# Performance work log

Hardware: AMD Instinct MI355X
Metric: run time of the kernel (lower is better)

Reference implementation:

```python
import jax, jax.numpy as jnp
import numpy as np

HEADS = 16
DIM_HEAD = 64
SCALE = DIM_HEAD ** -0.5


def setup_inputs() -> dict:
    key = jax.random.key(0)
    ks = jax.random.split(key, 5)
    dim = 1024
    inner = HEADS * DIM_HEAD  # 1024
    x = jax.random.normal(ks[0], (2, 2048, dim), dtype=jnp.float32)
    # Linear weights stored as [in, out] so y = x @ W
    s = dim ** -0.5
    Wq = jax.random.normal(ks[1], (dim, inner), dtype=jnp.float32) * s
    Wk = jax.random.normal(ks[2], (dim, inner), dtype=jnp.float32) * s
    Wv = jax.random.normal(ks[3], (dim, inner), dtype=jnp.float32) * s
    Wo = jax.random.normal(ks[4], (inner, dim), dtype=jnp.float32) * s
    bo = jnp.zeros((dim,), dtype=jnp.float32)
    return {"x": x, "Wq": Wq, "Wk": Wk, "Wv": Wv, "Wo": Wo, "bo": bo}


def reference(x, Wq, Wk, Wv, Wo, bo):
    b, n, _ = x.shape
    def split_heads(t):  # [b, n, h*d] -> [b, h, n, d]
        return t.reshape(b, n, HEADS, DIM_HEAD).transpose(0, 2, 1, 3)
    q = split_heads(x @ Wq)
    k = split_heads(x @ Wk)
    v = split_heads(x @ Wv)
    sim = jnp.einsum('bhid,bhjd->bhij', q, k) * SCALE  # [b, h, n, n]
    attn = jax.nn.softmax(sim, axis=-1)
    out = jnp.einsum('bhij,bhjd->bhid', attn, v)  # [b, h, n, d]
    out = out.transpose(0, 2, 1, 3).reshape(b, n, HEADS * DIM_HEAD)
    return out @ Wo + bo
```

## Files before the change

kernel.cpp:

```cpp
#include <hip/hip_runtime.h>
#include <hip/hip_fp16.h>

typedef _Float16 f16;
typedef __attribute__((ext_vector_type(8))) _Float16 half8;
typedef __attribute__((ext_vector_type(2))) __fp16 fp16x2_native;
typedef __attribute__((ext_vector_type(4))) float floatx4;
typedef __attribute__((ext_vector_type(16))) float f32x16;
typedef __attribute__((ext_vector_type(4))) unsigned uint4v;
typedef __attribute__((ext_vector_type(2))) unsigned uint2v;

static constexpr int DIM = 1024;
static constexpr int SEQ = 2048;
static constexpr int DH = 64;
static constexpr int MTOT = 4096;

__device__ __forceinline__ float fexp2(float x) {
#if __has_builtin(__builtin_amdgcn_exp2f)
  return __builtin_amdgcn_exp2f(x);
#else
  return exp2f(x);
#endif
}

__device__ __forceinline__ unsigned pkrtz(float a, float b) {
  fp16x2_native h = __builtin_amdgcn_cvt_pkrtz(a, b);
  return __builtin_bit_cast(unsigned, h);
}

__device__ __forceinline__ void pl32swap(unsigned& a, unsigned& b) {
#if __has_builtin(__builtin_amdgcn_permlane32_swap)
  uint2v r = __builtin_amdgcn_permlane32_swap(a, b, false, false);
  a = r.x;
  b = r.y;
#else
  asm volatile("v_permlane32_swap_b32 %0, %1" : "+v"(a), "+v"(b));
#endif
}

__device__ __forceinline__ void gll16(const f16* g, f16* l) {
  auto gp = (__attribute__((address_space(1))) unsigned*)(uintptr_t)(const void*)g;
  auto lp = (__attribute__((address_space(3))) unsigned*)(uintptr_t)(void*)l;
  __builtin_amdgcn_global_load_lds(gp, lp, 16, 0, 0);
}

__global__ __launch_bounds__(256) void k_transpose(
    const float* __restrict__ Wq, const float* __restrict__ Wk,
    const float* __restrict__ Wv, const float* __restrict__ Wo,
    f16* __restrict__ wt)
{
  __shared__ float tile[32][33];
  const int z = blockIdx.z;
  const float* W = (z == 0) ? Wq : (z == 1) ? Wk : (z == 2) ? Wv : Wo;
  f16* out = wt + (size_t)z * DIM * DIM;
  const int tx = threadIdx.x, ty = threadIdx.y;
  const int x0 = blockIdx.x * 32, y0 = blockIdx.y * 32;
#pragma unroll
  for (int i = 0; i < 4; ++i)
    tile[ty + i * 8][tx] = W[(size_t)(y0 + ty + i * 8) * DIM + (x0 + tx)];
  __syncthreads();
#pragma unroll
  for (int i = 0; i < 4; ++i)
    out[(size_t)(x0 + ty + i * 8) * DIM + (y0 + tx)] = (f16)tile[tx][ty + i * 8];
}

__global__ __launch_bounds__(256) void k_xcast(
    const float* __restrict__ in, f16* __restrict__ out)
{
  const int i = blockIdx.x * 256 + threadIdx.x;
  const float4* p = (const float4*)in;
  float4 a = p[2 * i], b = p[2 * i + 1];
  half8 h = {(f16)a.x, (f16)a.y, (f16)a.z, (f16)a.w,
             (f16)b.x, (f16)b.y, (f16)b.z, (f16)b.w};
  *(half8*)(out + (size_t)i * 8) = h;
}

__global__ __launch_bounds__(256) void k_vtrans(
    const f16* __restrict__ vh, f16* __restrict__ vt)
{
  __shared__ f16 T[64][72];
  const int tid = threadIdx.x;
  const int nt = blockIdx.x, bh = blockIdx.y;
  const int b = bh >> 4, h = bh & 15;
  const int n0 = nt * 64;
  const f16* src = vh + (size_t)b * SEQ * DIM + (size_t)h * DH;
#pragma unroll
  for (int i = 0; i < 2; ++i) {
    const int n = (tid >> 3) + i * 32;
    const int cc = tid & 7;
    half8 v = *(const half8*)(src + (size_t)(n0 + n) * DIM + cc * 8);
#pragma unroll
    for (int j = 0; j < 8; ++j) T[cc * 8 + j][n] = v[j];
  }
  __syncthreads();
  f16* dst = vt + (size_t)bh * DH * SEQ;
#pragma unroll
  for (int i = 0; i < 2; ++i) {
    const int d = (tid >> 3) + i * 32;
    const int cc = tid & 7;
    half8 w = *(const half8*)&T[d][cc * 8];
    *(half8*)(dst + (size_t)d * SEQ + n0 + cc * 8) = w;
  }
}

template <bool OUT_F32>
__global__ __launch_bounds__(256) void k_gemm2(
    const f16* __restrict__ A, const f16* __restrict__ BT,
    void* __restrict__ Cptr, const float* __restrict__ bias,
    int M, int N, int K, size_t bt_zstride, size_t c_zstride)
{
  __shared__ f16 SB[2][8192];

  const int tid = threadIdx.x;
  const int lane = tid & 63;
  const int wid = tid >> 6;
  const int wr = (wid >> 1) * 64, wc = (wid & 1) * 64;
  const int li = lane & 15, lg = lane >> 4;

  const f16* BTz = BT + (size_t)blockIdx.z * bt_zstride;
  const int row0 = blockIdx.x * 128, col0 = blockIdx.y * 128;

  const int c0 = tid;
  const int c1 = 256 + tid;
  const f16* a0 = A + (size_t)(row0 + (c0 >> 2)) * K + (c0 & 3) * 8;
  const f16* a1 = A + (size_t)(row0 + (c1 >> 2)) * K + (c1 & 3) * 8;
  const f16* b0 = BTz + (size_t)(col0 + (c0 >> 2)) * K + (c0 & 3) * 8;
  const f16* b1 = BTz + (size_t)(col0 + (c1 >> 2)) * K + (c1 & 3) * 8;
  const int da0 = wid * 512, da1 = 2048 + wid * 512;

  const floatx4 zero4 = {0.f, 0.f, 0.f, 0.f};
  floatx4 acc[4][4];
#pragma unroll
  for (int m = 0; m < 4; ++m)
#pragma unroll
    for (int n = 0; n < 4; ++n) acc[m][n] = zero4;

  auto issue = [&](int buf) {
    gll16(a0, &SB[buf][da0]);
    gll16(a1, &SB[buf][da1]);
    gll16(b0, &SB[buf][4096 + da0]);
    gll16(b1, &SB[buf][4096 + da1]);
    a0 += 32; a1 += 32; b0 += 32; b1 += 32;
  };

  const int nstep = K >> 5;
  issue(0);

  auto step = [&](int buf, int t) {
    asm volatile("s_waitcnt vmcnt(0)" ::: "memory");
    __builtin_amdgcn_s_barrier();
    asm volatile("" ::: "memory");
    if (t + 1 < nstep) issue(buf ^ 1);
    const f16* As = &SB[buf][0];
    const f16* Bs = &SB[buf][4096];
    half8 af[4], bf[4];
#pragma unroll
    for (int m = 0; m < 4; ++m)
      af[m] = *(const half8*)&As[(wr + m * 16 + li) * 32 + lg * 8];
#pragma unroll
    for (int n = 0; n < 4; ++n)
      bf[n] = *(const half8*)&Bs[(wc + n * 16 + li) * 32 + lg * 8];
#pragma unroll
    for (int m = 0; m < 4; ++m)
#pragma unroll
      for (int n = 0; n < 4; ++n)
        acc[m][n] = __builtin_amdgcn_mfma_f32_16x16x32_f16(af[m], bf[n], acc[m][n], 0, 0, 0);
  };

  for (int t2 = 0; t2 < nstep; t2 += 2) {
    step(0, t2);
    step(1, t2 + 1);
  }

#pragma unroll
  for (int m = 0; m < 4; ++m)
#pragma unroll
    for (int n = 0; n < 4; ++n)
#pragma unroll
      for (int r = 0; r < 4; ++r) {
        const int row = row0 + wr + m * 16 + lg * 4 + r;
        const int col = col0 + wc + n * 16 + li;
        if constexpr (OUT_F32) {
          float* C = (float*)Cptr + (size_t)blockIdx.z * c_zstride;
          C[(size_t)row * N + col] = acc[m][n][r] + bias[col];
        } else {
          f16* C = (f16*)Cptr + (size_t)blockIdx.z * c_zstride;
          C[(size_t)row * N + col] = (f16)acc[m][n][r];
        }
      }
}

__global__ __launch_bounds__(512) void k_attn4(
    const f16* __restrict__ qh, const f16* __restrict__ kh,
    const f16* __restrict__ vt, f16* __restrict__ oh)
{
  __shared__ f16 KV[2][16384];
  __shared__ float bc[8][32];
  __shared__ float Lm[4][32], Ll[4][32], W0[4][32], W1[4][32];

  const int tid = threadIdx.x;
  const int lane = tid & 63;
  const int wid = tid >> 6;
  const int g = wid >> 2;
  const int sub = wid & 3;
  const int col = lane & 31;
  const int hi = lane >> 5;

  const int id = blockIdx.x;
  const int xcd = id & 7;
  const int j = id >> 3;
  const int bh = xcd * 4 + (j >> 4);
  const int qi = j & 15;
  const int b = bh >> 4, h = bh & 15;

  const int q0 = qi * 128 + sub * 32;
  const size_t xbase = (size_t)b * SEQ * DIM + (size_t)h * DH;
  const size_t vtbase = (size_t)bh * DH * SEQ;

  const float SC = 0.125f * 1.44269504089f;
  const float RTRAW = 8.0f / SC;

  const int lc = tid & 511;
  const int srow = lc >> 3;
  const int sw = ((lc & 7) ^ (srow & 7)) * 8;
  const f16* ks0 = kh + xbase + (size_t)srow * DIM + sw;
  const f16* ks1 = kh + xbase + (size_t)(1024 + srow) * DIM + sw;
  const f16* vs0 = vt + vtbase + (size_t)srow * SEQ + sw;
  const f16* vs1 = vt + vtbase + (size_t)srow * SEQ + 1024 + sw;

  auto issue = [&](int buf) {
    f16* B = &KV[buf][wid * 512];
    gll16(ks0, B);
    gll16(vs0, B + 4096);
    gll16(ks1, B + 8192);
    gll16(vs1, B + 12288);
    ks0 += 64 * DIM; ks1 += 64 * DIM; vs0 += 64; vs1 += 64;
  };

  half8 qb[4];
  {
    const f16* qrow = qh + xbase + (size_t)(q0 + col) * DIM;
#pragma unroll
    for (int s = 0; s < 4; ++s) qb[s] = *(const half8*)(qrow + s * 16 + hi * 8);
  }

  f32x16 o0 = {0, 0, 0, 0, 0, 0, 0, 0, 0, 0, 0, 0, 0, 0, 0, 0};
  f32x16 o1 = {0, 0, 0, 0, 0, 0, 0, 0, 0, 0, 0, 0, 0, 0, 0, 0};
  float m = -1e30f, lsum = 0.f;

  issue(0);

  auto tile = [&](int buf, int t) {
    asm volatile("s_waitcnt vmcnt(0)" ::: "memory");
    __builtin_amdgcn_s_barrier();
    asm volatile("" ::: "memory");
    if (t < 15) issue(buf ^ 1);
    const f16* Ks = &KV[buf][g * 8192];
    const f16* Vs = Ks + 4096;

#pragma unroll
    for (int kvs = 0; kvs < 2; ++kvs) {
      const int krow = kvs * 32 + col;
      f32x16 sacc = {0, 0, 0, 0, 0, 0, 0, 0, 0, 0, 0, 0, 0, 0, 0, 0};
      __builtin_amdgcn_s_setprio(1);
#pragma unroll
      for (int s = 0; s < 4; ++s) {
        const int cc = (2 * s + hi) ^ (krow & 7);
        half8 ka = *(const half8*)&Ks[krow * 64 + cc * 8];
        sacc = __builtin_amdgcn_mfma_f32_32x32x16_f16(ka, qb[s], sacc, 0, 0, 0);
      }
      __builtin_amdgcn_s_setprio(0);

      float x0 = fmaxf(fmaxf(sacc[0], sacc[1]), fmaxf(sacc[2], sacc[3]));
      float x1 = fmaxf(fmaxf(sacc[4], sacc[5]), fmaxf(sacc[6], sacc[7]));
      float x2 = fmaxf(fmaxf(sacc[8], sacc[9]), fmaxf(sacc[10], sacc[11]));
      float x3 = fmaxf(fmaxf(sacc[12], sacc[13]), fmaxf(sacc[14], sacc[15]));
      float smax = fmaxf(fmaxf(x0, x1), fmaxf(x2, x3));
      smax = fmaxf(smax, __shfl_xor(smax, 32));

      if (!__all(smax <= m + RTRAW)) {
        const float mn = fmaxf(m, smax);
        const float alpha = fexp2((m - mn) * SC);
        m = mn;
        lsum *= alpha;
        if (hi == 0) bc[wid][col] = alpha;
#pragma unroll
        for (int r = 0; r < 16; ++r) {
          const float a2 = bc[wid][(r & 3) + 8 * (r >> 2) + 4 * hi];
          o0[r] *= a2;
          o1[r] *= a2;
        }
      }

      const float mc = m * SC;
      float pw[16];
#pragma unroll
      for (int r = 0; r < 16; ++r) pw[r] = fexp2(fmaf(sacc[r], SC, -mc));
      float s0 = (pw[0] + pw[1]) + (pw[2] + pw[3]);
      float s1 = (pw[4] + pw[5]) + (pw[6] + pw[7]);
      float s2 = (pw[8] + pw[9]) + (pw[10] + pw[11]);
      float s3 = (pw[12] + pw[13]) + (pw[14] + pw[15]);
      float rs = (s0 + s1) + (s2 + s3);
      rs += __shfl_xor(rs, 32);
      lsum += rs;

      __builtin_amdgcn_s_setprio(1);
#pragma unroll
      for (int s2i = 0; s2i < 2; ++s2i) {
        const int rb = s2i * 8;
        unsigned X0 = pkrtz(pw[rb + 0], pw[rb + 1]);
        unsigned X1 = pkrtz(pw[rb + 2], pw[rb + 3]);
        unsigned Y0 = pkrtz(pw[rb + 4], pw[rb + 5]);
        unsigned Y1 = pkrtz(pw[rb + 6], pw[rb + 7]);
        pl32swap(X0, Y0);
        pl32swap(X1, Y1);
        const half8 paf = __builtin_bit_cast(half8, (uint4v){X0, X1, Y0, Y1});
        const int kc = kvs * 4 + s2i * 2 + hi;
#pragma unroll
        for (int dt = 0; dt < 2; ++dt) {
          const int vrow = dt * 32 + col;
          const int cc = kc ^ (vrow & 7);
          half8 vb = *(const half8*)&Vs[vrow * 64 + cc * 8];
          if (dt == 0)
            o0 = __builtin_amdgcn_mfma_f32_32x32x16_f16(paf, vb, o0, 0, 0, 0);
          else
            o1 = __builtin_amdgcn_mfma_f32_32x32x16_f16(paf, vb, o1, 0, 0, 0);
        }
      }
      __builtin_amdgcn_s_setprio(0);
    }
  };

  for (int t2 = 0; t2 < 16; t2 += 2) {
    tile(0, t2);
    tile(1, t2 + 1);
  }

  const float inv = 1.0f / lsum;
  if (hi == 0) bc[wid][col] = inv;
  if (g == 1) {
    if (hi == 0) { Lm[sub][col] = m; Ll[sub][col] = lsum; }
    f16* po = &KV[0][0] + sub * 2048;
#pragma unroll
    for (int r = 0; r < 16; ++r) {
      const int qr = (r & 3) + 8 * (r >> 2) + 4 * hi;
      const float iv = bc[wid][qr];
      po[qr * 64 + col] = (f16)(o0[r] * iv);
      po[qr * 64 + 32 + col] = (f16)(o1[r] * iv);
    }
  }
  __syncthreads();
  if (g == 0) {
    const float m1 = Lm[sub][col], l1 = Ll[sub][col];
    const float M = fmaxf(m, m1);
    const float e0 = fexp2((m - M) * SC);
    const float a0 = lsum * e0;
    const float a1 = l1 * fexp2((m1 - M) * SC);
    const float rden = 1.0f / (a0 + a1);
    const float c0 = e0 * rden;
    const float w1 = a1 * rden;
    if (hi == 0) { W0[sub][col] = c0; W1[sub][col] = w1; }
    const f16* po = &KV[0][0] + sub * 2048;
#pragma unroll
    for (int r = 0; r < 16; ++r) {
      const int qr = (r & 3) + 8 * (r >> 2) + 4 * hi;
      const float c0r = W0[sub][qr], w1r = W1[sub][qr];
      f16* orow = oh + xbase + (size_t)(q0 + qr) * DIM;
      orow[col] = (f16)(c0r * o0[r] + w1r * (float)po[qr * 64 + col]);
      orow[32 + col] = (f16)(c0r * o1[r] + w1r * (float)po[qr * 64 + 32 + col]);
    }
  }
}

extern "C" void kernel_launch(void* const* d_in, const int* in_sizes, int n_in,
                              void* d_out, int out_size, void* d_ws, size_t ws_size,
                              hipStream_t stream)
{
  const float* x  = (const float*)d_in[0];
  const float* Wq = (const float*)d_in[1];
  const float* Wk = (const float*)d_in[2];
  const float* Wv = (const float*)d_in[3];
  const float* Wo = (const float*)d_in[4];
  const float* bo = (const float*)d_in[5];

  char* ws = (char*)d_ws;
  f16* wt   = (f16*)ws;
  f16* qkvh = (f16*)(ws + (size_t)8 * 1024 * 1024);
  f16* ohp  = (f16*)(ws + (size_t)32 * 1024 * 1024);
  f16* vtb  = (f16*)(ws + (size_t)40 * 1024 * 1024);
  f16* xh   = ohp;

  k_transpose<<<dim3(32, 32, 4), dim3(32, 8), 0, stream>>>(Wq, Wk, Wv, Wo, wt);

  k_xcast<<<2048, 256, 0, stream>>>(x, xh);

  k_gemm2<false><<<dim3(32, 8, 3), 256, 0, stream>>>(
      xh, wt, qkvh, nullptr, MTOT, DIM, DIM,
      (size_t)DIM * DIM, (size_t)MTOT * DIM);

  k_vtrans<<<dim3(32, 32), 256, 0, stream>>>(
      qkvh + (size_t)2 * MTOT * DIM, vtb);

  k_attn4<<<512, 512, 0, stream>>>(
      qkvh, qkvh + (size_t)MTOT * DIM, vtb, ohp);

  k_gemm2<true><<<dim3(32, 8, 1), 256, 0, stream>>>(
      ohp, wt + (size_t)3 * DIM * DIM, d_out, bo, MTOT, DIM, DIM, 0, 0);
}
```

Baseline: 120.7 us.

## Batch QK MFMAs per tile and use a wave-uniform running max

Both 32-key QK^T MFMA chains of a tile are issued back to back before either softmax step, so the second chain's matrix work can overlap the exp and PV processing of the first. The running max becomes wave-uniform through a full xor-shuffle reduction, so the rescale multiplies by a scalar alpha and no longer goes through LDS. Exponentials are computed speculatively with the old max and recomputed only when the max grows, and the row-sum cross-half shuffle moves out of the loop to the end. In exchange it holds an extra accumulator (more VGPRs), and the coarser shared max may raise the rescale rate or lose a little precision.

```diff
diff --git a/kernel.cpp b/kernel.cpp
--- a/kernel.cpp
+++ b/kernel.cpp
@@ -189,7 +189,7 @@
       }
 }
 
-__global__ __launch_bounds__(512) void k_attn4(
+__global__ __launch_bounds__(512) void k_attn7(
     const f16* __restrict__ qh, const f16* __restrict__ kh,
     const f16* __restrict__ vt, f16* __restrict__ oh)
 {
@@ -245,9 +245,68 @@
 
   f32x16 o0 = {0, 0, 0, 0, 0, 0, 0, 0, 0, 0, 0, 0, 0, 0, 0, 0};
   f32x16 o1 = {0, 0, 0, 0, 0, 0, 0, 0, 0, 0, 0, 0, 0, 0, 0, 0};
-  float m = -1e30f, lsum = 0.f;
+  float m = -1e30f, mc = 0.f;
+  float lsum = 0.f;
 
   issue(0);
+
+  auto process = [&](const f32x16& sacc, int kvs, const f16* Vs) {
+    float pw[16];
+#pragma unroll
+    for (int r = 0; r < 16; ++r) pw[r] = fexp2(fmaf(sacc[r], SC, -mc));
+
+    float x0 = fmaxf(fmaxf(sacc[0], sacc[1]), fmaxf(sacc[2], sacc[3]));
+    float x1 = fmaxf(fmaxf(sacc[4], sacc[5]), fmaxf(sacc[6], sacc[7]));
+    float x2 = fmaxf(fmaxf(sacc[8], sacc[9]), fmaxf(sacc[10], sacc[11]));
+    float x3 = fmaxf(fmaxf(sacc[12], sacc[13]), fmaxf(sacc[14], sacc[15]));
+    const float smax = fmaxf(fmaxf(x0, x1), fmaxf(x2, x3));
+
+    if (!__all(smax <= m + RTRAW)) {
+      float wm = smax;
+#pragma unroll
+      for (int off = 1; off < 64; off <<= 1) wm = fmaxf(wm, __shfl_xor(wm, off));
+      const float mn = fmaxf(m, wm);
+      const float alpha = fexp2((m - mn) * SC);
+      m = mn;
+      mc = m * SC;
+      lsum *= alpha;
+#pragma unroll
+      for (int r = 0; r < 16; ++r) { o0[r] *= alpha; o1[r] *= alpha; }
+#pragma unroll
+      for (int r = 0; r < 16; ++r) pw[r] = fexp2(fmaf(sacc[r], SC, -mc));
+    }
+
+    float t0 = (pw[0] + pw[1]) + (pw[2] + pw[3]);
+    float t1 = (pw[4] + pw[5]) + (pw[6] + pw[7]);
+    float t2 = (pw[8] + pw[9]) + (pw[10] + pw[11]);
+    float t3 = (pw[12] + pw[13]) + (pw[14] + pw[15]);
+    lsum += (t0 + t1) + (t2 + t3);
+
+    __builtin_amdgcn_s_setprio(1);
+#pragma unroll
+    for (int s2i = 0; s2i < 2; ++s2i) {
+      const int rb = s2i * 8;
+      unsigned X0 = pkrtz(pw[rb + 0], pw[rb + 1]);
+      unsigned X1 = pkrtz(pw[rb + 2], pw[rb + 3]);
+      unsigned Y0 = pkrtz(pw[rb + 4], pw[rb + 5]);
+      unsigned Y1 = pkrtz(pw[rb + 6], pw[rb + 7]);
+      pl32swap(X0, Y0);
+      pl32swap(X1, Y1);
+      const half8 paf = __builtin_bit_cast(half8, (uint4v){X0, X1, Y0, Y1});
+      const int kc = kvs * 4 + s2i * 2 + hi;
+#pragma unroll
+      for (int dt = 0; dt < 2; ++dt) {
+        const int vrow = dt * 32 + col;
+        const int cc = kc ^ (vrow & 7);
+        half8 vb = *(const half8*)&Vs[vrow * 64 + cc * 8];
+        if (dt == 0)
+          o0 = __builtin_amdgcn_mfma_f32_32x32x16_f16(paf, vb, o0, 0, 0, 0);
+        else
+          o1 = __builtin_amdgcn_mfma_f32_32x32x16_f16(paf, vb, o1, 0, 0, 0);
+      }
+    }
+    __builtin_amdgcn_s_setprio(0);
+  };
 
   auto tile = [&](int buf, int t) {
     asm volatile("s_waitcnt vmcnt(0)" ::: "memory");
@@ -257,77 +316,26 @@
     const f16* Ks = &KV[buf][g * 8192];
     const f16* Vs = Ks + 4096;
 
-#pragma unroll
-    for (int kvs = 0; kvs < 2; ++kvs) {
-      const int krow = kvs * 32 + col;
-      f32x16 sacc = {0, 0, 0, 0, 0, 0, 0, 0, 0, 0, 0, 0, 0, 0, 0, 0};
-      __builtin_amdgcn_s_setprio(1);
-#pragma unroll
-      for (int s = 0; s < 4; ++s) {
-        const int cc = (2 * s + hi) ^ (krow & 7);
-        half8 ka = *(const half8*)&Ks[krow * 64 + cc * 8];
-        sacc = __builtin_amdgcn_mfma_f32_32x32x16_f16(ka, qb[s], sacc, 0, 0, 0);
-      }
-      __builtin_amdgcn_s_setprio(0);
-
-      float x0 = fmaxf(fmaxf(sacc[0], sacc[1]), fmaxf(sacc[2], sacc[3]));
-      float x1 = fmaxf(fmaxf(sacc[4], sacc[5]), fmaxf(sacc[6], sacc[7]));
-      float x2 = fmaxf(fmaxf(sacc[8], sacc[9]), fmaxf(sacc[10], sacc[11]));
-      float x3 = fmaxf(fmaxf(sacc[12], sacc[13]), fmaxf(sacc[14], sacc[15]));
-      float smax = fmaxf(fmaxf(x0, x1), fmaxf(x2, x3));
-      smax = fmaxf(smax, __shfl_xor(smax, 32));
-
-      if (!__all(smax <= m + RTRAW)) {
-        const float mn = fmaxf(m, smax);
-        const float alpha = fexp2((m - mn) * SC);
-        m = mn;
-        lsum *= alpha;
-        if (hi == 0) bc[wid][col] = alpha;
-#pragma unroll
-        for (int r = 0; r < 16; ++r) {
-          const float a2 = bc[wid][(r & 3) + 8 * (r >> 2) + 4 * hi];
-          o0[r] *= a2;
-          o1[r] *= a2;
-        }
-      }
-
-      const float mc = m * SC;
-      float pw[16];
-#pragma unroll
-      for (int r = 0; r < 16; ++r) pw[r] = fexp2(fmaf(sacc[r], SC, -mc));
-      float s0 = (pw[0] + pw[1]) + (pw[2] + pw[3]);
-      float s1 = (pw[4] + pw[5]) + (pw[6] + pw[7]);
-      float s2 = (pw[8] + pw[9]) + (pw[10] + pw[11]);
-      float s3 = (pw[12] + pw[13]) + (pw[14] + pw[15]);
-      float rs = (s0 + s1) + (s2 + s3);
-      rs += __shfl_xor(rs, 32);
-      lsum += rs;
-
-      __builtin_amdgcn_s_setprio(1);
-#pragma unroll
-      for (int s2i = 0; s2i < 2; ++s2i) {
-        const int rb = s2i * 8;
-        unsigned X0 = pkrtz(pw[rb + 0], pw[rb + 1]);
-        unsigned X1 = pkrtz(pw[rb + 2], pw[rb + 3]);
-        unsigned Y0 = pkrtz(pw[rb + 4], pw[rb + 5]);
-        unsigned Y1 = pkrtz(pw[rb + 6], pw[rb + 7]);
-        pl32swap(X0, Y0);
-        pl32swap(X1, Y1);
-        const half8 paf = __builtin_bit_cast(half8, (uint4v){X0, X1, Y0, Y1});
-        const int kc = kvs * 4 + s2i * 2 + hi;
-#pragma unroll
-        for (int dt = 0; dt < 2; ++dt) {
-          const int vrow = dt * 32 + col;
-          const int cc = kc ^ (vrow & 7);
-          half8 vb = *(const half8*)&Vs[vrow * 64 + cc * 8];
-          if (dt == 0)
-            o0 = __builtin_amdgcn_mfma_f32_32x32x16_f16(paf, vb, o0, 0, 0, 0);
-          else
-            o1 = __builtin_amdgcn_mfma_f32_32x32x16_f16(paf, vb, o1, 0, 0, 0);
-        }
-      }
-      __builtin_amdgcn_s_setprio(0);
-    }
+    f32x16 sa = {0, 0, 0, 0, 0, 0, 0, 0, 0, 0, 0, 0, 0, 0, 0, 0};
+    f32x16 sb = {0, 0, 0, 0, 0, 0, 0, 0, 0, 0, 0, 0, 0, 0, 0, 0};
+    __builtin_amdgcn_s_setprio(1);
+#pragma unroll
+    for (int s = 0; s < 4; ++s) {
+      const int cc = (2 * s + hi) ^ (col & 7);
+      half8 ka = *(const half8*)&Ks[col * 64 + cc * 8];
+      sa = __builtin_amdgcn_mfma_f32_32x32x16_f16(ka, qb[s], sa, 0, 0, 0);
+    }
+#pragma unroll
+    for (int s = 0; s < 4; ++s) {
+      const int krow = 32 + col;
+      const int cc = (2 * s + hi) ^ (krow & 7);
+      half8 ka = *(const half8*)&Ks[krow * 64 + cc * 8];
+      sb = __builtin_amdgcn_mfma_f32_32x32x16_f16(ka, qb[s], sb, 0, 0, 0);
+    }
+    __builtin_amdgcn_s_setprio(0);
+
+    process(sa, 0, Vs);
+    process(sb, 1, Vs);
   };
 
   for (int t2 = 0; t2 < 16; t2 += 2) {
@@ -335,10 +343,11 @@
     tile(1, t2 + 1);
   }
 
-  const float inv = 1.0f / lsum;
-  if (hi == 0) bc[wid][col] = inv;
+  lsum += __shfl_xor(lsum, 32);
+
   if (g == 1) {
-    if (hi == 0) { Lm[sub][col] = m; Ll[sub][col] = lsum; }
+    const float inv = 1.0f / lsum;
+    if (hi == 0) { Lm[sub][col] = m; Ll[sub][col] = lsum; bc[wid][col] = inv; }
     f16* po = &KV[0][0] + sub * 2048;
 #pragma unroll
     for (int r = 0; r < 16; ++r) {
@@ -400,7 +409,7 @@
   k_vtrans<<<dim3(32, 32), 256, 0, stream>>>(
       qkvh + (size_t)2 * MTOT * DIM, vtb);
 
-  k_attn4<<<512, 512, 0, stream>>>(
+  k_attn7<<<512, 512, 0, stream>>>(
       qkvh, qkvh + (size_t)MTOT * DIM, vtb, ohp);
 
   k_gemm2<true><<<dim3(32, 8, 1), 256, 0, stream>>>(
```

After: 122.6 us. Within noise of the previous version (+1.5%).
